# Kernel tuning notes

Measured on AMD Instinct MI355X. Metric: run time of the kernel, lower is better.

Reference implementation:

```python
import jax, jax.numpy as jnp
import numpy as np

V, E, N, H, L = 50257, 768, 1024, 12, 6
HD = E // H
FF = 4 * E
B = 2


def sinusoidal_pos(n, dim):
    # Faithful to populate_sinusoidal_pos_emb: interleaved sin/cos with the
    # torch code's (slightly nonstandard) cos exponent 2*arange(1,dim,2)/dim.
    pos = jnp.arange(n, dtype=jnp.float32)[:, None]
    i = jnp.arange(0, dim, 2, dtype=jnp.float32)
    j = jnp.arange(1, dim, 2, dtype=jnp.float32)
    s = jnp.sin(pos / jnp.power(10000.0, 2.0 * i / dim))  # [n, dim/2]
    c = jnp.cos(pos / jnp.power(10000.0, 2.0 * j / dim))  # [n, dim/2]
    return jnp.stack([s, c], axis=-1).reshape(n, dim)


def gelu(x):
    # tanh-approximation GELU (custom gelu.GELU in the repo)
    return 0.5 * x * (1.0 + jnp.tanh(jnp.sqrt(2.0 / jnp.pi) * (x + 0.044715 * x * x * x)))


def layer_norm(x, g, b, eps=1e-5):
    mu = jnp.mean(x, axis=-1, keepdims=True)
    var = jnp.var(x, axis=-1, keepdims=True)  # biased, matches unbiased=False
    return g * (x - mu) / jnp.sqrt(var + eps) + b


def setup_inputs() -> dict:
    key = jax.random.key(0)
    ks = jax.random.split(key, 12)
    s = 0.02
    inp = {
        "x": jax.random.randint(ks[0], (B, N), 0, V),
        "tok_emb": s * jax.random.normal(ks[1], (V, E), dtype=jnp.float32),
        "wq": s * jax.random.normal(ks[2], (L, E, E), dtype=jnp.float32),
        "wk": s * jax.random.normal(ks[3], (L, E, E), dtype=jnp.float32),
        "wv": s * jax.random.normal(ks[4], (L, E, E), dtype=jnp.float32),
        "wo": s * jax.random.normal(ks[5], (L, E, E), dtype=jnp.float32),
        "bo": jnp.zeros((L, E), dtype=jnp.float32),
        "ln1_g": jnp.ones((L, E), dtype=jnp.float32),
        "ln1_b": jnp.zeros((L, E), dtype=jnp.float32),
        "ln2_g": jnp.ones((L, E), dtype=jnp.float32),
        "ln2_b": jnp.zeros((L, E), dtype=jnp.float32),
        "w1": s * jax.random.normal(ks[6], (L, E, FF), dtype=jnp.float32),
        "b1": jnp.zeros((L, FF), dtype=jnp.float32),
        "w2": s * jax.random.normal(ks[7], (L, FF, E), dtype=jnp.float32),
        "b2": jnp.zeros((L, E), dtype=jnp.float32),
        "lnf_g": jnp.ones((E,), dtype=jnp.float32),
        "lnf_b": jnp.zeros((E,), dtype=jnp.float32),
        "w_head": s * jax.random.normal(ks[8], (E, V), dtype=jnp.float32),
    }
    return inp


def reference(x, tok_emb, wq, wk, wv, wo, bo, ln1_g, ln1_b, ln2_g, ln2_b,
              w1, b1, w2, b2, lnf_g, lnf_b, w_head):
    b, n = x.shape
    h = tok_emb[x] + sinusoidal_pos(n, E)  # [B, N, E]; dropout is identity (p=0)
    causal = jnp.triu(jnp.ones((n, n), dtype=bool), k=1)  # True above diagonal
    scale = HD ** 0.5
    for l in range(L):
        # attention sub-block
        y = layer_norm(h, ln1_g[l], ln1_b[l])
        q = (y @ wq[l]).reshape(b, n, H, HD).transpose(0, 2, 1, 3)  # [B,H,N,HD]
        k = (y @ wk[l]).reshape(b, n, H, HD).transpose(0, 2, 1, 3)
        v = (y @ wv[l]).reshape(b, n, H, HD).transpose(0, 2, 1, 3)
        attn = jnp.einsum('bhqd,bhkd->bhqk', q, k)  # [B,H,N,N]
        attn = jnp.where(causal, -jnp.inf, attn) / scale  # mask before scale, as in source
        attn = jax.nn.softmax(attn, axis=-1)
        o = jnp.einsum('bhqk,bhkd->bhqd', attn, v)
        o = o.transpose(0, 2, 1, 3).reshape(b, n, E) @ wo[l] + bo[l]
        h = h + o
        # FFN sub-block
        y = layer_norm(h, ln2_g[l], ln2_b[l])
        y = gelu(y @ w1[l] + b1[l]) @ w2[l] + b2[l]
        h = h + y
    h = layer_norm(h, lnf_g, lnf_b)
    return h @ w_head  # [B, N, V]
```

## Files before the change

kernel.cpp:

```cpp
#include <hip/hip_runtime.h>
#include <hip/hip_bf16.h>
#include <math.h>

#define B_  2
#define N_  1024
#define E_  768
#define H_  12
#define HD_ 64
#define L_  6
#define FF_ 3072
#define V_  50257
#define VPAD_ 50304
#define QKVW_ 2304
#define M_  (B_ * N_)

#define OFF_QKV_ 0
#define OFF_WO_  (QKVW_ * E_)
#define OFF_W1_  (OFF_WO_ + E_ * E_)
#define OFF_W2_  (OFF_W1_ + FF_ * E_)
#define WSLAB_   ((size_t)(OFF_W2_ + E_ * FF_))

typedef short short8 __attribute__((ext_vector_type(8)));
typedef float f32x4 __attribute__((ext_vector_type(4)));

__device__ __forceinline__ float gelu_f(float x) {
  return 0.5f * x * (1.0f + tanhf(0.7978845608028654f * (x + 0.044715f * x * x * x)));
}

__device__ __forceinline__ unsigned short f2bf(float f) {
  __hip_bfloat16 b = __float2bfloat16(f);
  return *reinterpret_cast<unsigned short*>(&b);
}

__device__ __forceinline__ void async_ld16(const void* g, void* l) {
  __builtin_amdgcn_global_load_lds(
      (const __attribute__((address_space(1))) void*)g,
      (__attribute__((address_space(3))) void*)l, 16, 0, 0);
}

__global__ __launch_bounds__(256) void embed_kernel(const int* __restrict__ x,
    const float* __restrict__ tok, float* __restrict__ h) {
  int idx = blockIdx.x * 256 + threadIdx.x;
  const int total = B_ * N_ * E_;
  if (idx >= total) return;
  int e  = idx % E_;
  int bn = idx / E_;
  int n  = bn % N_;
  int t  = x[bn];
  float freq = expf(-9.210340371976184f * (float)(2 * e) / (float)E_);
  float arg  = (float)n * freq;
  float pe   = (e & 1) ? cosf(arg) : sinf(arg);
  h[idx] = tok[(size_t)t * E_ + e] + pe;
}

__global__ __launch_bounds__(256) void layernorm_kernel(const float* __restrict__ in,
    __hip_bfloat16* __restrict__ out, const float* __restrict__ g, const float* __restrict__ b) {
  int row = blockIdx.x;
  const float* xr = in + (size_t)row * E_;
  __shared__ float red[256];
  int tid = threadIdx.x;
  float s = 0.f, ss = 0.f;
  for (int e = tid; e < E_; e += 256) { float v = xr[e]; s += v; ss += v * v; }
  red[tid] = s; __syncthreads();
  for (int o = 128; o > 0; o >>= 1) { if (tid < o) red[tid] += red[tid + o]; __syncthreads(); }
  float mean = red[0] / (float)E_;
  __syncthreads();
  red[tid] = ss; __syncthreads();
  for (int o = 128; o > 0; o >>= 1) { if (tid < o) red[tid] += red[tid + o]; __syncthreads(); }
  float var = red[0] / (float)E_ - mean * mean;
  float inv = rsqrtf(var + 1e-5f);
  for (int e = tid; e < E_; e += 256)
    out[(size_t)row * E_ + e] = __float2bfloat16(g[e] * (xr[e] - mean) * inv + b[e]);
}

__global__ __launch_bounds__(256) void transpose_cast_kernel(const float* __restrict__ in,
    __hip_bfloat16* __restrict__ out, int K, int Nn) {
  __shared__ float t[64][65];
  int k0 = blockIdx.x * 64, n0 = blockIdx.y * 64;
  int tid = threadIdx.x;
  int c = tid & 63, rg = tid >> 6;
#pragma unroll
  for (int i = 0; i < 16; ++i) {
    int r = rg * 16 + i;
    int n = n0 + c;
    t[r][c] = (n < Nn) ? in[(size_t)(k0 + r) * Nn + n] : 0.0f;
  }
  __syncthreads();
#pragma unroll
  for (int i = 0; i < 16; ++i) {
    int ro = rg * 16 + i;
    out[(size_t)(n0 + ro) * K + (k0 + c)] = __float2bfloat16(t[c][ro]);
  }
}

__global__ __launch_bounds__(256) void wtrans_kernel(
    const float* __restrict__ wq, const float* __restrict__ wk,
    const float* __restrict__ wv, const float* __restrict__ wo,
    const float* __restrict__ w1, const float* __restrict__ w2,
    __hip_bfloat16* __restrict__ out, int l0) {
  int bid = blockIdx.x;
  int lay = bid / 1728;
  int t = bid - lay * 1728;
  int lsrc = l0 + lay;
  __hip_bfloat16* ob = out + (size_t)lay * WSLAB_;
  const float* src; __hip_bfloat16* dst;
  int K, Nn, ntk;
  if (t < 576) {
    int which = t / 144; t -= which * 144;
    K = E_; Nn = E_; ntk = 12;
    if (which == 0)      { src = wq + (size_t)lsrc * E_ * E_; dst = ob + OFF_QKV_; }
    else if (which == 1) { src = wk + (size_t)lsrc * E_ * E_; dst = ob + OFF_QKV_ + (size_t)E_ * E_; }
    else if (which == 2) { src = wv + (size_t)lsrc * E_ * E_; dst = ob + OFF_QKV_ + (size_t)2 * E_ * E_; }
    else                 { src = wo + (size_t)lsrc * E_ * E_; dst = ob + OFF_WO_; }
  } else if (t < 1152) {
    t -= 576; K = E_; Nn = FF_; ntk = 12;
    src = w1 + (size_t)lsrc * E_ * FF_; dst = ob + OFF_W1_;
  } else {
    t -= 1152; K = FF_; Nn = E_; ntk = 48;
    src = w2 + (size_t)lsrc * FF_ * E_; dst = ob + OFF_W2_;
  }
  int kt = t % ntk, nt = t / ntk;
  int k0 = kt * 64, n0 = nt * 64;
  __shared__ float tt[64][65];
  int tid = threadIdx.x;
  int c = tid & 63, rg = tid >> 6;
#pragma unroll
  for (int i = 0; i < 16; ++i) {
    int r = rg * 16 + i;
    tt[r][c] = src[(size_t)(k0 + r) * Nn + n0 + c];
  }
  __syncthreads();
#pragma unroll
  for (int i = 0; i < 16; ++i) {
    int ro = rg * 16 + i;
    dst[(size_t)(n0 + ro) * K + (k0 + c)] = __float2bfloat16(tt[c][ro]);
  }
}

template<int BM>
__global__ __launch_bounds__(256) void gemm_bt_kernel(
    const __hip_bfloat16* __restrict__ A, const __hip_bfloat16* __restrict__ Bt,
    const float* __restrict__ bias, const float* __restrict__ R,
    float* __restrict__ Cf, __hip_bfloat16* __restrict__ Cb,
    __hip_bfloat16* __restrict__ vt,
    int Nn, int K, int flags, int nrt) {
  constexpr int NROWS = BM + 64;
  constexpr int WRT = BM / 4;
  constexpr int MF  = WRT / 16;
  __shared__ __align__(16) unsigned short SM[2 * NROWS * 64];
  int tid = threadIdx.x;
  int w = tid >> 6, l = tid & 63;
  int bx, by;
  if (nrt > 0) {
    int bid = blockIdx.x;
    int q = gridDim.x >> 3;
    int nb = (bid & 7) * q + (bid >> 3);
    bx = nb / nrt; by = nb - bx * nrt;
  } else { bx = blockIdx.x; by = blockIdx.y; }
  int row0 = by * BM, col0 = bx * 64;
  int lr = l & 15, kg = l >> 4;
  const unsigned short* Ag = (const unsigned short*)A;
  const unsigned short* Bg = (const unsigned short*)Bt;
  int srow = l >> 3;
  int schunk = (l & 7) ^ srow;

  constexpr int NS = NROWS / 32;
  constexpr int A8 = BM / 8;
  auto stage = [&](int buf, int k0) {
    unsigned short* As = SM + buf * (NROWS * 64);
    unsigned short* Bs = As + BM * 64;
#pragma unroll
    for (int s = 0; s < NS; ++s) {
      int idx8 = s * 4 + w;
      if (idx8 < A8)
        async_ld16(Ag + (size_t)(row0 + idx8 * 8 + srow) * K + k0 + schunk * 8,
                   &As[idx8 * 8 * 64]);
      else
        async_ld16(Bg + (size_t)(col0 + (idx8 - A8) * 8 + srow) * K + k0 + schunk * 8,
                   &Bs[(idx8 - A8) * 8 * 64]);
    }
  };

  f32x4 acc[MF][4];
#pragma unroll
  for (int m = 0; m < MF; ++m)
#pragma unroll
    for (int n = 0; n < 4; ++n) acc[m][n] = (f32x4){0.f, 0.f, 0.f, 0.f};

  int nt = K >> 6;
  stage(0, 0);
  __syncthreads();
  int cur = 0;
  for (int t = 0; t < nt; ++t) {
    if (t + 1 < nt) stage(cur ^ 1, (t + 1) << 6);
    const unsigned short* As = SM + cur * (NROWS * 64);
    const unsigned short* Bs = As + BM * 64;
#pragma unroll
    for (int hf = 0; hf < 2; ++hf) {
      short8 af[MF], bf[4];
#pragma unroll
      for (int m = 0; m < MF; ++m) {
        int r = w * WRT + m * 16 + lr;
        af[m] = *(const short8*)&As[r * 64 + ((((hf << 2) | kg)) ^ (lr & 7)) * 8];
      }
#pragma unroll
      for (int n = 0; n < 4; ++n) {
        int r = n * 16 + lr;
        bf[n] = *(const short8*)&Bs[r * 64 + ((((hf << 2) | kg)) ^ (lr & 7)) * 8];
      }
#pragma unroll
      for (int m = 0; m < MF; ++m)
#pragma unroll
        for (int n = 0; n < 4; ++n)
          acc[m][n] = __builtin_amdgcn_mfma_f32_16x16x32_bf16(af[m], bf[n], acc[m][n], 0, 0, 0);
    }
    if (t + 1 < nt) { __syncthreads(); cur ^= 1; }
  }

  if (flags & 2) {
    float* Ls = (float*)SM;
    __syncthreads();
#pragma unroll
    for (int m = 0; m < MF; ++m)
#pragma unroll
      for (int n = 0; n < 4; ++n)
#pragma unroll
        for (int j = 0; j < 4; ++j) {
          int r = w * WRT + m * 16 + kg * 4 + j;
          int c = n * 16 + lr;
          Ls[r * 64 + (c ^ (16 * (kg & 1)))] = acc[m][n][j];
        }
    __syncthreads();
    bool nfull = (col0 + 64 <= Nn);
    constexpr int ITER = BM * 64 / 256;
#pragma unroll
    for (int i = 0; i < ITER; ++i) {
      int idx = i * 256 + tid;
      int r = idx >> 6, c = idx & 63;
      float v = Ls[r * 64 + (c ^ (16 * ((r >> 2) & 1)))];
      if (nfull || col0 + c < Nn)
        __builtin_nontemporal_store(v, &Cf[(size_t)(row0 + r) * Nn + col0 + c]);
    }
    return;
  }

  unsigned short* vtb = (unsigned short*)vt;
#pragma unroll
  for (int n = 0; n < 4; ++n) {
    int col = col0 + n * 16 + lr;
    if (col >= Nn) continue;
    float bv = bias ? bias[col] : 0.f;
    bool to_vt = (vtb != nullptr) && (col >= 2 * E_);
    int hh = 0, dd = 0;
    if (to_vt) { int c2 = col - 2 * E_; hh = c2 >> 6; dd = c2 & 63; }
#pragma unroll
    for (int m = 0; m < MF; ++m) {
#pragma unroll
      for (int j = 0; j < 4; ++j) {
        int row = row0 + w * WRT + m * 16 + kg * 4 + j;
        float val = acc[m][n][j] + bv;
        if (flags & 1) val = gelu_f(val);
        if (R) val += R[(size_t)row * Nn + col];
        if (Cf) Cf[(size_t)row * Nn + col] = val;
        if (to_vt) {
          int bz = row >> 10, nn = row & (N_ - 1);
          vtb[((size_t)(bz * H_ + hh) * HD_ + dd) * N_ + nn] = f2bf(val);
        } else if (Cb) {
          Cb[(size_t)row * Nn + col] = __float2bfloat16(val);
        }
      }
    }
  }
}

#define PRS_ 40
__global__ __launch_bounds__(64) void fattn_kernel(
    const __hip_bfloat16* __restrict__ qkv, const __hip_bfloat16* __restrict__ vt,
    __hip_bfloat16* __restrict__ o) {
  int qt = blockIdx.x, hh = blockIdx.y, bz = blockIdx.z;
  int q0 = qt * 16;
  int l = threadIdx.x;
  int lr = l & 15, kg = l >> 4;
  const unsigned short* base = (const unsigned short*)qkv;
  const unsigned short* vtb = (const unsigned short*)vt + ((size_t)(bz * H_ + hh)) * HD_ * N_;
  __shared__ __align__(16) unsigned short P[16 * PRS_];

  short8 qf[2];
  const unsigned short* qrow = base + (size_t)(bz * N_ + q0 + lr) * QKVW_ + hh * HD_;
#pragma unroll
  for (int c = 0; c < 2; ++c) qf[c] = *(const short8*)(qrow + c * 32 + kg * 8);

  float mrow[4], lsum[4];
  f32x4 accO[4];
#pragma unroll
  for (int j = 0; j < 4; ++j) { mrow[j] = -INFINITY; lsum[j] = 0.f; }
#pragma unroll
  for (int db = 0; db < 4; ++db) accO[db] = (f32x4){0.f, 0.f, 0.f, 0.f};

  int nsteps = (q0 + 16 + 31) / 32;
  for (int kt = 0; kt < nsteps; ++kt) {
    f32x4 s[2];
#pragma unroll
    for (int t = 0; t < 2; ++t) {
      const unsigned short* krow = base + (size_t)(bz * N_ + kt * 32 + t * 16 + lr) * QKVW_ + E_ + hh * HD_;
      short8 kf0 = *(const short8*)(krow + kg * 8);
      short8 kf1 = *(const short8*)(krow + 32 + kg * 8);
      f32x4 acc = (f32x4){0.f, 0.f, 0.f, 0.f};
      acc = __builtin_amdgcn_mfma_f32_16x16x32_bf16(qf[0], kf0, acc, 0, 0, 0);
      acc = __builtin_amdgcn_mfma_f32_16x16x32_bf16(qf[1], kf1, acc, 0, 0, 0);
      s[t] = acc;
    }
    float pm[2][4];
#pragma unroll
    for (int t = 0; t < 2; ++t) {
      int kglob = kt * 32 + t * 16 + lr;
#pragma unroll
      for (int j = 0; j < 4; ++j) {
        int qglob = q0 + kg * 4 + j;
        pm[t][j] = (kglob <= qglob) ? s[t][j] * 0.125f : -INFINITY;
      }
    }
#pragma unroll
    for (int j = 0; j < 4; ++j) {
      float tm = fmaxf(pm[0][j], pm[1][j]);
      tm = fmaxf(tm, __shfl_xor(tm, 1));
      tm = fmaxf(tm, __shfl_xor(tm, 2));
      tm = fmaxf(tm, __shfl_xor(tm, 4));
      tm = fmaxf(tm, __shfl_xor(tm, 8));
      float mnew = fmaxf(mrow[j], tm);
      float alpha = __expf(mrow[j] - mnew);
      float p0 = __expf(pm[0][j] - mnew);
      float p1 = __expf(pm[1][j] - mnew);
      float rs = p0 + p1;
      rs += __shfl_xor(rs, 1);
      rs += __shfl_xor(rs, 2);
      rs += __shfl_xor(rs, 4);
      rs += __shfl_xor(rs, 8);
      lsum[j] = lsum[j] * alpha + rs;
      mrow[j] = mnew;
#pragma unroll
      for (int db = 0; db < 4; ++db) accO[db][j] *= alpha;
      P[(kg * 4 + j) * PRS_ + lr]      = f2bf(p0);
      P[(kg * 4 + j) * PRS_ + 16 + lr] = f2bf(p1);
    }
    __syncthreads();
    short8 pa = *(const short8*)&P[lr * PRS_ + kg * 8];
#pragma unroll
    for (int db = 0; db < 4; ++db) {
      short8 vf = *(const short8*)(vtb + (size_t)(db * 16 + lr) * N_ + kt * 32 + kg * 8);
      accO[db] = __builtin_amdgcn_mfma_f32_16x16x32_bf16(pa, vf, accO[db], 0, 0, 0);
    }
    __syncthreads();
  }
  unsigned short* ob = (unsigned short*)o;
#pragma unroll
  for (int j = 0; j < 4; ++j) {
    float inv = 1.f / lsum[j];
    size_t orow = (size_t)(bz * N_ + q0 + kg * 4 + j) * E_ + hh * HD_;
#pragma unroll
    for (int db = 0; db < 4; ++db)
      ob[orow + db * 16 + lr] = f2bf(accO[db][j] * inv);
  }
}

extern "C" void kernel_launch(void* const* d_in, const int* in_sizes, int n_in,
                              void* d_out, int out_size, void* d_ws, size_t ws_size,
                              hipStream_t stream) {
  const int*   x     = (const int*)  d_in[0];
  const float* tok   = (const float*)d_in[1];
  const float* wq    = (const float*)d_in[2];
  const float* wk    = (const float*)d_in[3];
  const float* wv    = (const float*)d_in[4];
  const float* wo    = (const float*)d_in[5];
  const float* bo    = (const float*)d_in[6];
  const float* ln1g  = (const float*)d_in[7];
  const float* ln1b  = (const float*)d_in[8];
  const float* ln2g  = (const float*)d_in[9];
  const float* ln2b  = (const float*)d_in[10];
  const float* w1    = (const float*)d_in[11];
  const float* b1    = (const float*)d_in[12];
  const float* w2    = (const float*)d_in[13];
  const float* b2    = (const float*)d_in[14];
  const float* lnfg  = (const float*)d_in[15];
  const float* lnfb  = (const float*)d_in[16];
  const float* whead = (const float*)d_in[17];
  float* out = (float*)d_out;

  char* wsb = (char*)d_ws;
  size_t off = 0;
  auto alloc = [&](size_t bytes) -> void* {
    void* p = wsb + off; off += (bytes + 255) & ~(size_t)255; return p;
  };
  float*           h        = (float*)          alloc((size_t)M_ * E_ * 4);
  __hip_bfloat16*  y_bf     = (__hip_bfloat16*) alloc((size_t)M_ * E_ * 2);
  __hip_bfloat16*  qkv_bf   = (__hip_bfloat16*) alloc((size_t)M_ * QKVW_ * 2);
  __hip_bfloat16*  vt_bf    = (__hip_bfloat16*) alloc((size_t)B_ * H_ * HD_ * N_ * 2);
  __hip_bfloat16*  o_bf     = (__hip_bfloat16*) alloc((size_t)M_ * E_ * 2);
  __hip_bfloat16*  mid_bf   = (__hip_bfloat16*) alloc((size_t)M_ * FF_ * 2);
  __hip_bfloat16*  whead_bt = (__hip_bfloat16*) alloc((size_t)VPAD_ * E_ * 2);
  bool preall = (off + (size_t)6 * WSLAB_ * 2 <= ws_size);
  __hip_bfloat16* wslab = (__hip_bfloat16*) alloc(((size_t)(preall ? 6 : 1)) * WSLAB_ * 2);

  dim3 blk(256);

  embed_kernel<<<(B_ * N_ * E_ + 255) / 256, blk, 0, stream>>>(x, tok, h);
  transpose_cast_kernel<<<dim3(E_ / 64, VPAD_ / 64), blk, 0, stream>>>(whead, whead_bt, E_, V_);
  if (preall)
    wtrans_kernel<<<6 * 1728, blk, 0, stream>>>(wq, wk, wv, wo, w1, w2, wslab, 0);

  dim3 gqkv(QKVW_ / 64, M_ / 128);
  dim3 gffn1(FF_ / 64, M_ / 128);
  dim3 gsm(E_ / 64, M_ / 64);
  dim3 gfa(N_ / 16, H_, B_);

  for (int l = 0; l < L_; ++l) {
    if (!preall)
      wtrans_kernel<<<1728, blk, 0, stream>>>(wq, wk, wv, wo, w1, w2, wslab, l);
    __hip_bfloat16* wb = wslab + (preall ? (size_t)l * WSLAB_ : 0);

    layernorm_kernel<<<M_, blk, 0, stream>>>(h, y_bf, ln1g + (size_t)l * E_, ln1b + (size_t)l * E_);
    gemm_bt_kernel<128><<<gqkv, blk, 0, stream>>>(y_bf, wb + OFF_QKV_, nullptr, nullptr,
        nullptr, qkv_bf, vt_bf, QKVW_, E_, 0, 0);
    fattn_kernel<<<gfa, dim3(64), 0, stream>>>(qkv_bf, vt_bf, o_bf);
    gemm_bt_kernel<64><<<gsm, blk, 0, stream>>>(o_bf, wb + OFF_WO_, bo + (size_t)l * E_, h,
        h, nullptr, nullptr, E_, E_, 0, 0);
    layernorm_kernel<<<M_, blk, 0, stream>>>(h, y_bf, ln2g + (size_t)l * E_, ln2b + (size_t)l * E_);
    gemm_bt_kernel<128><<<gffn1, blk, 0, stream>>>(y_bf, wb + OFF_W1_, b1 + (size_t)l * FF_,
        nullptr, nullptr, mid_bf, nullptr, FF_, E_, 1, 0);
    gemm_bt_kernel<64><<<gsm, blk, 0, stream>>>(mid_bf, wb + OFF_W2_, b2 + (size_t)l * E_, h,
        h, nullptr, nullptr, E_, FF_, 0, 0);
  }

  layernorm_kernel<<<M_, blk, 0, stream>>>(h, y_bf, lnfg, lnfb);
  gemm_bt_kernel<128><<<dim3((VPAD_ / 64) * (M_ / 128)), blk, 0, stream>>>(
      y_bf, whead_bt, nullptr, nullptr, out, nullptr, nullptr, V_, E_, 2, M_ / 128);
}
```

Before: 1.431 ms.

## Add dedicated 128x128-tile LM-head GEMM kernel with staged epilogue

Moves the vocabulary projection out of the generic GEMM into a dedicated kernel. The new kernel uses 128x128 output tiles with a 2x2 warp layout and a K-step of 32. It writes the fp32 output through shared memory in four 32-row passes using nontemporal stores. The larger square tile roughly doubles operand reuse per loaded byte on the largest GEMM, which is mostly bound by its output write. In exchange the grid has fewer blocks, there are more epilogue barriers, and the main loop uses a shorter K-step with more synchronisation per FLOP.

```diff
diff --git a/kernel.cpp b/kernel.cpp
--- a/kernel.cpp
+++ b/kernel.cpp
@@ -143,20 +143,14 @@
     const float* __restrict__ bias, const float* __restrict__ R,
     float* __restrict__ Cf, __hip_bfloat16* __restrict__ Cb,
     __hip_bfloat16* __restrict__ vt,
-    int Nn, int K, int flags, int nrt) {
+    int Nn, int K, int flags) {
   constexpr int NROWS = BM + 64;
   constexpr int WRT = BM / 4;
   constexpr int MF  = WRT / 16;
   __shared__ __align__(16) unsigned short SM[2 * NROWS * 64];
   int tid = threadIdx.x;
   int w = tid >> 6, l = tid & 63;
-  int bx, by;
-  if (nrt > 0) {
-    int bid = blockIdx.x;
-    int q = gridDim.x >> 3;
-    int nb = (bid & 7) * q + (bid >> 3);
-    bx = nb / nrt; by = nb - bx * nrt;
-  } else { bx = blockIdx.x; by = blockIdx.y; }
+  int bx = blockIdx.x, by = blockIdx.y;
   int row0 = by * BM, col0 = bx * 64;
   int lr = l & 15, kg = l >> 4;
   const unsigned short* Ag = (const unsigned short*)A;
@@ -215,33 +209,6 @@
           acc[m][n] = __builtin_amdgcn_mfma_f32_16x16x32_bf16(af[m], bf[n], acc[m][n], 0, 0, 0);
     }
     if (t + 1 < nt) { __syncthreads(); cur ^= 1; }
-  }
-
-  if (flags & 2) {
-    float* Ls = (float*)SM;
-    __syncthreads();
-#pragma unroll
-    for (int m = 0; m < MF; ++m)
-#pragma unroll
-      for (int n = 0; n < 4; ++n)
-#pragma unroll
-        for (int j = 0; j < 4; ++j) {
-          int r = w * WRT + m * 16 + kg * 4 + j;
-          int c = n * 16 + lr;
-          Ls[r * 64 + (c ^ (16 * (kg & 1)))] = acc[m][n][j];
-        }
-    __syncthreads();
-    bool nfull = (col0 + 64 <= Nn);
-    constexpr int ITER = BM * 64 / 256;
-#pragma unroll
-    for (int i = 0; i < ITER; ++i) {
-      int idx = i * 256 + tid;
-      int r = idx >> 6, c = idx & 63;
-      float v = Ls[r * 64 + (c ^ (16 * ((r >> 2) & 1)))];
-      if (nfull || col0 + c < Nn)
-        __builtin_nontemporal_store(v, &Cf[(size_t)(row0 + r) * Nn + col0 + c]);
-    }
-    return;
   }
 
   unsigned short* vtb = (unsigned short*)vt;
@@ -267,6 +234,108 @@
           vtb[((size_t)(bz * H_ + hh) * HD_ + dd) * N_ + nn] = f2bf(val);
         } else if (Cb) {
           Cb[(size_t)row * Nn + col] = __float2bfloat16(val);
+        }
+      }
+    }
+  }
+}
+
+__global__ __launch_bounds__(256) void head_gemm_kernel(
+    const __hip_bfloat16* __restrict__ A, const __hip_bfloat16* __restrict__ Bt,
+    float* __restrict__ Cf, int Nn, int K, int nrt) {
+  __shared__ __align__(16) unsigned short SM[2 * 256 * 32];
+  int tid = threadIdx.x;
+  int w = tid >> 6, l = tid & 63;
+  int wr = w >> 1, wc = w & 1;
+  int bid = blockIdx.x;
+  int q = gridDim.x >> 3;
+  int nb = (bid & 7) * q + (bid >> 3);
+  int bx = nb / nrt, by = nb - bx * nrt;
+  int row0 = by * 128, col0 = bx * 128;
+  int lr = l & 15, kg = l >> 4;
+  const unsigned short* Ag = (const unsigned short*)A;
+  const unsigned short* Bg = (const unsigned short*)Bt;
+  int srow = l >> 2;
+  int schunk = (l & 3) ^ (l >> 4);
+
+  auto stage = [&](int buf, int k0) {
+    unsigned short* As = SM + buf * (256 * 32);
+    unsigned short* Bs = As + 128 * 32;
+#pragma unroll
+    for (int s = 0; s < 4; ++s) {
+      int g = s * 4 + w;
+      if (g < 8)
+        async_ld16(Ag + (size_t)(row0 + g * 16 + srow) * K + k0 + schunk * 8,
+                   &As[g * 16 * 32]);
+      else
+        async_ld16(Bg + (size_t)(col0 + (g - 8) * 16 + srow) * K + k0 + schunk * 8,
+                   &Bs[(g - 8) * 16 * 32]);
+    }
+  };
+
+  f32x4 acc[4][4];
+#pragma unroll
+  for (int m = 0; m < 4; ++m)
+#pragma unroll
+    for (int n = 0; n < 4; ++n) acc[m][n] = (f32x4){0.f, 0.f, 0.f, 0.f};
+
+  int rchunk = (kg ^ ((lr >> 2) & 3)) * 8;
+  int nt = K >> 5;
+  stage(0, 0);
+  __syncthreads();
+  int cur = 0;
+  for (int t = 0; t < nt; ++t) {
+    if (t + 1 < nt) stage(cur ^ 1, (t + 1) << 5);
+    const unsigned short* As = SM + cur * (256 * 32);
+    const unsigned short* Bs = As + 128 * 32;
+    short8 af[4], bf[4];
+#pragma unroll
+    for (int m = 0; m < 4; ++m)
+      af[m] = *(const short8*)&As[(wr * 64 + m * 16 + lr) * 32 + rchunk];
+#pragma unroll
+    for (int n = 0; n < 4; ++n)
+      bf[n] = *(const short8*)&Bs[(wc * 64 + n * 16 + lr) * 32 + rchunk];
+#pragma unroll
+    for (int m = 0; m < 4; ++m)
+#pragma unroll
+      for (int n = 0; n < 4; ++n)
+        acc[m][n] = __builtin_amdgcn_mfma_f32_16x16x32_bf16(af[m], bf[n], acc[m][n], 0, 0, 0);
+    if (t + 1 < nt) { __syncthreads(); cur ^= 1; }
+  }
+
+  float* Ls = (float*)SM;
+  bool nfull = (col0 + 128 <= Nn);
+#pragma unroll
+  for (int p = 0; p < 4; ++p) {
+    __syncthreads();
+    if (wr == (p >> 1)) {
+      int mb = (p & 1) * 2;
+#pragma unroll
+      for (int m2 = 0; m2 < 2; ++m2)
+#pragma unroll
+        for (int n = 0; n < 4; ++n)
+#pragma unroll
+          for (int j = 0; j < 4; ++j)
+            Ls[(m2 * 16 + kg * 4 + j) * 128 + ((wc * 64 + n * 16 + lr) ^ (16 * (kg & 1)))]
+                = acc[mb + m2][n][j];
+    }
+    __syncthreads();
+    int rbase = row0 + p * 32;
+    if (nfull) {
+#pragma unroll
+      for (int i = 0; i < 16; ++i) {
+        int idx = i * 256 + tid;
+        int r = idx >> 7, c = idx & 127;
+        float v = Ls[r * 128 + (c ^ (16 * ((r >> 2) & 1)))];
+        __builtin_nontemporal_store(v, &Cf[(size_t)(rbase + r) * Nn + col0 + c]);
+      }
+    } else {
+      for (int i = 0; i < 16; ++i) {
+        int idx = i * 256 + tid;
+        int r = idx >> 7, c = idx & 127;
+        if (col0 + c < Nn) {
+          float v = Ls[r * 128 + (c ^ (16 * ((r >> 2) & 1)))];
+          __builtin_nontemporal_store(v, &Cf[(size_t)(rbase + r) * Nn + col0 + c]);
         }
       }
     }
@@ -420,18 +489,18 @@
 
     layernorm_kernel<<<M_, blk, 0, stream>>>(h, y_bf, ln1g + (size_t)l * E_, ln1b + (size_t)l * E_);
     gemm_bt_kernel<128><<<gqkv, blk, 0, stream>>>(y_bf, wb + OFF_QKV_, nullptr, nullptr,
-        nullptr, qkv_bf, vt_bf, QKVW_, E_, 0, 0);
+        nullptr, qkv_bf, vt_bf, QKVW_, E_, 0);
     fattn_kernel<<<gfa, dim3(64), 0, stream>>>(qkv_bf, vt_bf, o_bf);
     gemm_bt_kernel<64><<<gsm, blk, 0, stream>>>(o_bf, wb + OFF_WO_, bo + (size_t)l * E_, h,
-        h, nullptr, nullptr, E_, E_, 0, 0);
+        h, nullptr, nullptr, E_, E_, 0);
     layernorm_kernel<<<M_, blk, 0, stream>>>(h, y_bf, ln2g + (size_t)l * E_, ln2b + (size_t)l * E_);
     gemm_bt_kernel<128><<<gffn1, blk, 0, stream>>>(y_bf, wb + OFF_W1_, b1 + (size_t)l * FF_,
-        nullptr, nullptr, mid_bf, nullptr, FF_, E_, 1, 0);
+        nullptr, nullptr, mid_bf, nullptr, FF_, E_, 1);
     gemm_bt_kernel<64><<<gsm, blk, 0, stream>>>(mid_bf, wb + OFF_W2_, b2 + (size_t)l * E_, h,
-        h, nullptr, nullptr, E_, FF_, 0, 0);
+        h, nullptr, nullptr, E_, FF_, 0);
   }
 
   layernorm_kernel<<<M_, blk, 0, stream>>>(h, y_bf, lnfg, lnfb);
-  gemm_bt_kernel<128><<<dim3((VPAD_ / 64) * (M_ / 128)), blk, 0, stream>>>(
-      y_bf, whead_bt, nullptr, nullptr, out, nullptr, nullptr, V_, E_, 2, M_ / 128);
-}
+  head_gemm_kernel<<<dim3((VPAD_ / 128) * (M_ / 128)), blk, 0, stream>>>(
+      y_bf, whead_bt, out, V_, E_, M_ / 128);
+}
```

New measurement: 1.337 ms. 1.07x faster.
